# Kernel optimization log

Hardware: AMD Instinct MI355X
Metric: run time of the kernel (lower is better)

Reference implementation:

```python
import jax, jax.numpy as jnp
import numpy as np

K = 4  # neighbors per node (init kwarg)


def setup_inputs() -> dict:
    key = jax.random.key(0)
    node_features = jax.random.normal(key, (8, 4096, 256), dtype=jnp.float32)
    return {"node_features": node_features}


def reference(node_features):
    # node_features: (B, N, C)
    B, N, C = node_features.shape
    k = min(K, N - 1)
    # cosine metric: L2-normalize rows, then pairwise dot products
    fn = node_features / jnp.linalg.norm(node_features, axis=-1, keepdims=True)
    sim = jnp.einsum("bnc,bmc->bnm", fn, fn)  # (B, N, N)
    # exclude self-loops: fill diagonal with -inf
    diag = jnp.eye(N, dtype=bool)
    sim = jnp.where(diag[None, :, :], -jnp.inf, sim)
    topk_values, topk_indices = jax.lax.top_k(sim, k)  # (B, N, k)
    # edge list per batch: source i repeated k times, target = topk index
    src = jnp.broadcast_to(jnp.arange(N)[:, None], (N, k)).reshape(-1)  # (N*k,)
    src = jnp.broadcast_to(src[None, :], (B, N * k))
    tgt = topk_indices.reshape(B, N * k)
    edge_index = jnp.stack([src, tgt], axis=1)  # (B, 2, N*k)
    edge_weight = topk_values.reshape(B, N * k)  # (B, N*k)
    return edge_index, edge_weight
```

## Files before the change

### kernel.cpp

```cpp
#include <hip/hip_runtime.h>
#include <hip/hip_bf16.h>
#include <float.h>
#include <limits.h>

#define BATCH 8
#define NN    4096
#define CC    256
#define KNN_K 4
#define NKE   (NN * KNN_K)

#define MTI  64
#define NJ   64
#define NC8  8
#define NM6  6
#define BROW 264

typedef __attribute__((ext_vector_type(8))) short  bf16x8;
typedef __attribute__((ext_vector_type(4))) float  f32x4;

__device__ __forceinline__ short f2bf(float f) {
    unsigned u = __float_as_uint(f);
    return (short)((u + 0x7FFFu + ((u >> 16) & 1u)) >> 16);
}

__device__ __forceinline__ unsigned umin32(unsigned a, unsigned b) { return a < b ? a : b; }
__device__ __forceinline__ unsigned umax32(unsigned a, unsigned b) { return a > b ? a : b; }

__device__ __forceinline__ void pk_ins8(unsigned k, unsigned (&t)[NC8]) {
    #pragma unroll
    for (int s = NC8 - 1; s > 0; --s) t[s] = umax32(t[s], umin32(t[s - 1], k));
    t[0] = umax32(t[0], k);
}
__device__ __forceinline__ void pk_ins6(unsigned k, unsigned (&t)[NM6]) {
    #pragma unroll
    for (int s = NM6 - 1; s > 0; --s) t[s] = umax32(t[s], umin32(t[s - 1], k));
    t[0] = umax32(t[0], k);
}

__device__ __forceinline__ bool knn_better(float v, int j, float v2, int j2) {
    return (v > v2) || (v == v2 && j < j2);
}
__device__ __forceinline__ void knn_insert4(float v, int j, float (&tv)[4], int (&tj)[4]) {
    if (knn_better(v, j, tv[3], tj[3])) {
        tv[3] = v; tj[3] = j;
        #pragma unroll
        for (int s = 3; s > 0; --s) {
            if (knn_better(tv[s], tj[s], tv[s - 1], tj[s - 1])) {
                float fv = tv[s]; tv[s] = tv[s - 1]; tv[s - 1] = fv;
                int   fj = tj[s]; tj[s] = tj[s - 1]; tj[s - 1] = fj;
            }
        }
    }
}

__global__ void knn_prep_kernel(const float* __restrict__ x, float* __restrict__ invn,
                                ushort* __restrict__ xn, int write_bf16) {
    const int row  = blockIdx.x * 4 + (threadIdx.x >> 6);
    const int lane = threadIdx.x & 63;
    const float4 v = *(const float4*)(x + (size_t)row * CC + lane * 4);
    float ss = v.x * v.x + v.y * v.y + v.z * v.z + v.w * v.w;
    #pragma unroll
    for (int off = 32; off > 0; off >>= 1) ss += __shfl_down(ss, off, 64);
    const float inv = 1.0f / sqrtf(__shfl(ss, 0, 64));
    if (lane == 0) invn[row] = inv;
    if (write_bf16) {
        short4 s4;
        s4.x = f2bf(v.x * inv); s4.y = f2bf(v.y * inv);
        s4.z = f2bf(v.z * inv); s4.w = f2bf(v.w * inv);
        *(short4*)(xn + (size_t)row * CC + lane * 4) = s4;
    }
}

template<bool FROM_BF16>
__global__ __launch_bounds__(256, 3) void knn_main_kernel(
        const float* __restrict__ x, const float* __restrict__ invn,
        const ushort* __restrict__ xn, float* __restrict__ out,
        float* __restrict__ sval, int* __restrict__ sjid, int nh2) {
    __shared__ __align__(16) ushort Bsh[NJ * BROW];

    const int tid = threadIdx.x;
    const int b   = blockIdx.x & 7;
    const int t   = blockIdx.x >> 3;
    const int it   = nh2 ? (t >> 1) : t;
    const int half = nh2 ? (t & 1)  : 0;
    const int i0   = it * MTI;
    const int jbase = half * (NN / 2);
    const int nch   = nh2 ? (NN / NJ / 2) : (NN / NJ);

    const float*  xb   = x    + (size_t)b * NN * CC;
    const ushort* xnb  = xn   + (size_t)b * NN * CC;
    const float*  invb = invn + (size_t)b * NN;

    const int w  = tid >> 6;
    const int l  = tid & 63;
    const int lm = l & 15;
    const int q  = l >> 4;

    bf16x8 afrag[8];
    const int gi = i0 + w * 16 + lm;
    if (FROM_BF16) {
        #pragma unroll
        for (int kt = 0; kt < 8; ++kt)
            afrag[kt] = *(const bf16x8*)(xnb + (size_t)gi * CC + kt * 32 + q * 8);
    } else {
        const float vi = invb[gi];
        #pragma unroll
        for (int kt = 0; kt < 8; ++kt) {
            const float* src = xb + (size_t)gi * CC + kt * 32 + q * 8;
            const float4 f0 = *(const float4*)(src);
            const float4 f1 = *(const float4*)(src + 4);
            bf16x8 a;
            a[0] = f2bf(f0.x * vi); a[1] = f2bf(f0.y * vi);
            a[2] = f2bf(f0.z * vi); a[3] = f2bf(f0.w * vi);
            a[4] = f2bf(f1.x * vi); a[5] = f2bf(f1.y * vi);
            a[6] = f2bf(f1.z * vi); a[7] = f2bf(f1.w * vi);
            afrag[kt] = a;
        }
    }

    unsigned cl[4][NC8];
    #pragma unroll
    for (int r = 0; r < 4; ++r)
        #pragma unroll
        for (int s = 0; s < NC8; ++s) cl[r][s] = 0u;

    const int s_gc = tid & 31;
    const int s_r0 = tid >> 5;
    bf16x8 pregs[8];
    if (FROM_BF16) {
        #pragma unroll
        for (int lp = 0; lp < 8; ++lp)
            pregs[lp] = *(const bf16x8*)(xnb + (size_t)(jbase + s_r0 + 8 * lp) * CC + s_gc * 8);
    }

    for (int jt = 0; jt < nch; ++jt) {
        const int j0 = jbase + jt * NJ;
        __syncthreads();
        if (FROM_BF16) {
            #pragma unroll
            for (int lp = 0; lp < 8; ++lp)
                *(bf16x8*)(Bsh + (s_r0 + 8 * lp) * BROW + s_gc * 8) = pregs[lp];
        } else {
            #pragma unroll
            for (int lp = 0; lp < 16; ++lp) {
                const int u2 = tid + 256 * lp;
                const int row = u2 >> 6, c4 = u2 & 63;
                const float sc = invb[j0 + row];
                const float4 v = *(const float4*)(xb + (size_t)(j0 + row) * CC + c4 * 4);
                short4 s4;
                s4.x = f2bf(v.x * sc); s4.y = f2bf(v.y * sc);
                s4.z = f2bf(v.z * sc); s4.w = f2bf(v.w * sc);
                *(short4*)(Bsh + row * BROW + c4 * 4) = s4;
            }
        }
        __syncthreads();
        if (FROM_BF16 && jt + 1 < nch) {
            const int jn = jbase + (jt + 1) * NJ;
            #pragma unroll
            for (int lp = 0; lp < 8; ++lp)
                pregs[lp] = *(const bf16x8*)(xnb + (size_t)(jn + s_r0 + 8 * lp) * CC + s_gc * 8);
        }

        f32x4 acc[4];
        #pragma unroll
        for (int ct = 0; ct < 4; ++ct) acc[ct] = (f32x4){0.f, 0.f, 0.f, 0.f};
        #pragma unroll
        for (int kt = 0; kt < 8; ++kt) {
            #pragma unroll
            for (int ct = 0; ct < 4; ++ct) {
                const bf16x8 bf = *(const bf16x8*)(Bsh + (ct * 16 + lm) * BROW + kt * 32 + q * 8);
                acc[ct] = __builtin_amdgcn_mfma_f32_16x16x32_bf16(afrag[kt], bf, acc[ct], 0, 0, 0);
            }
        }

        const bool dchunk = (j0 == i0);
        #pragma unroll
        for (int ct = 0; ct < 4; ++ct) {
            const int jg  = j0 + ct * 16 + lm;
            const unsigned ivj = (unsigned)(4095 - jg);
            #pragma unroll
            for (int r = 0; r < 4; ++r) {
                unsigned pk = (__float_as_uint(acc[ct][r] + 2.0f) & 0xFFFFF000u) | ivj;
                if (dchunk && (w * 16 + q * 4 + r) == (ct * 16 + lm)) pk = 0u;
                pk_ins8(pk, cl[r]);
            }
        }
    }

    unsigned tm[4][NM6];
    #pragma unroll
    for (int r = 0; r < 4; ++r)
        #pragma unroll
        for (int s = 0; s < NM6; ++s) tm[r][s] = cl[r][s];
    #pragma unroll
    for (int m = 1; m <= 8; m <<= 1) {
        #pragma unroll
        for (int r = 0; r < 4; ++r) {
            unsigned pin[NM6];
            #pragma unroll
            for (int s = 0; s < NM6; ++s)
                pin[s] = (unsigned)__shfl_xor((int)tm[r][s], m, 64);
            #pragma unroll
            for (int s = 0; s < NM6; ++s) pk_ins6(pin[s], tm[r]);
        }
    }

    unsigned* cpk = (unsigned*)Bsh;
    __syncthreads();
    if (lm == 0) {
        #pragma unroll
        for (int r = 0; r < 4; ++r) {
            const int rt = w * 16 + q * 4 + r;
            #pragma unroll
            for (int s = 0; s < NM6; ++s) cpk[rt * NM6 + s] = tm[r][s];
        }
    }
    __syncthreads();

    const int rr   = tid & 63;
    const int slot = tid >> 6;
    const int ig   = i0 + rr;
    const float inv_i = invb[ig];
    const float* xi = xb + (size_t)ig * CC;
    const int ncand = (slot < 2) ? 2 : 1;
    const int cbase = (slot < 2) ? slot * 2 : 2 + slot;
    float rv[2]; int rj[2];
    for (int u = 0; u < ncand; ++u) {
        const int c  = cbase + u;
        const int jc = 4095 - (int)(cpk[rr * NM6 + c] & 0xFFFu);
        const float* xj = xb + (size_t)jc * CC;
        float d = 0.f;
        #pragma unroll 16
        for (int k4 = 0; k4 < 64; ++k4) {
            const float4 av = *(const float4*)(xi + k4 * 4);
            const float4 bv = *(const float4*)(xj + k4 * 4);
            d = fmaf(av.x, bv.x, d);
            d = fmaf(av.y, bv.y, d);
            d = fmaf(av.z, bv.z, d);
            d = fmaf(av.w, bv.w, d);
        }
        rv[u] = d * inv_i * invb[jc];
        rj[u] = jc;
    }

    if (nh2) {
        for (int u = 0; u < ncand; ++u) {
            const size_t o = ((size_t)(b * NN + ig) * 2 + half) * NM6 + (cbase + u);
            sval[o] = rv[u];
            sjid[o] = rj[u];
        }
        return;
    }

    float* cvl = (float*)(Bsh + 4096);
    for (int u = 0; u < ncand; ++u) cvl[rr * NM6 + (cbase + u)] = rv[u];
    __syncthreads();
    if (tid < MTI) {
        const int r = tid, ig2 = i0 + r;
        float fv[4]; int fj[4];
        #pragma unroll
        for (int s = 0; s < 4; ++s) { fv[s] = -INFINITY; fj[s] = INT_MAX; }
        for (int c = 0; c < NM6; ++c) {
            const int jc = 4095 - (int)(cpk[r * NM6 + c] & 0xFFFu);
            knn_insert4(cvl[r * NM6 + c], jc, fv, fj);
        }
        float* o_src = out + (size_t)b * 2 * NKE;
        float* o_tgt = o_src + NKE;
        float* o_w   = out + (size_t)BATCH * 2 * NKE + (size_t)b * NKE;
        #pragma unroll
        for (int s = 0; s < 4; ++s) {
            o_src[ig2 * KNN_K + s] = (float)ig2;
            o_tgt[ig2 * KNN_K + s] = (float)fj[s];
            o_w[ig2 * KNN_K + s]   = fv[s];
        }
    }
}

__global__ __launch_bounds__(256) void knn_select_kernel(
        const float* __restrict__ sval, const int* __restrict__ sjid,
        float* __restrict__ out) {
    const int row_g = blockIdx.x * 256 + threadIdx.x;
    const int bb = row_g >> 12, ig = row_g & (NN - 1);
    float fv[4]; int fj[4];
    #pragma unroll
    for (int s = 0; s < 4; ++s) { fv[s] = -INFINITY; fj[s] = INT_MAX; }
    const size_t base = (size_t)row_g * 2 * NM6;
    for (int c = 0; c < 2 * NM6; ++c)
        knn_insert4(sval[base + c], sjid[base + c], fv, fj);
    float* o_src = out + (size_t)bb * 2 * NKE;
    float* o_tgt = o_src + NKE;
    float* o_w   = out + (size_t)BATCH * 2 * NKE + (size_t)bb * NKE;
    #pragma unroll
    for (int s = 0; s < 4; ++s) {
        o_src[ig * KNN_K + s] = (float)ig;
        o_tgt[ig * KNN_K + s] = (float)fj[s];
        o_w[ig * KNN_K + s]   = fv[s];
    }
}

extern "C" void kernel_launch(void* const* d_in, const int* in_sizes, int n_in,
                              void* d_out, int out_size, void* d_ws, size_t ws_size,
                              hipStream_t stream) {
    const float* x    = (const float*)d_in[0];
    float*       out  = (float*)d_out;
    float*       invn = (float*)d_ws;
    ushort*      xn   = (ushort*)((char*)d_ws + 131072);
    char*        p2   = (char*)d_ws + 131072 + (size_t)BATCH * NN * CC * sizeof(ushort);
    float*       sval = (float*)p2;
    int*         sjid = (int*)(p2 + (size_t)BATCH * NN * 2 * NM6 * sizeof(float));
    const size_t need_xn  = 131072 + (size_t)BATCH * NN * CC * sizeof(ushort);
    const size_t need_all = need_xn + (size_t)BATCH * NN * 2 * NM6 * 8;

    if (ws_size >= need_all) {
        knn_prep_kernel<<<(BATCH * NN) / 4, 256, 0, stream>>>(x, invn, xn, 1);
        knn_main_kernel<true><<<BATCH * MTI * 2, 256, 0, stream>>>(x, invn, xn, out, sval, sjid, 1);
        knn_select_kernel<<<(BATCH * NN) / 256, 256, 0, stream>>>(sval, sjid, out);
    } else if (ws_size >= need_xn) {
        knn_prep_kernel<<<(BATCH * NN) / 4, 256, 0, stream>>>(x, invn, xn, 1);
        knn_main_kernel<true><<<BATCH * MTI, 256, 0, stream>>>(x, invn, xn, out, nullptr, nullptr, 0);
    } else {
        knn_prep_kernel<<<(BATCH * NN) / 4, 256, 0, stream>>>(x, invn, xn, 0);
        knn_main_kernel<false><<<BATCH * MTI, 256, 0, stream>>>(x, invn, xn, out, nullptr, nullptr, 0);
    }
}
```

Before: 256.4 us.

## Use 2x2 wave tiling with direct global-to-LDS loads and per-half candidate lists

Each wave now computes a 32x32 sub-tile of the 64x64 similarity block instead of 16x64. This halves the B-fragment LDS reads per MFMA by reusing each B fragment across two A row tiles. The B tile is filled with global_load_lds straight into shared memory, replacing the register prefetch and LDS store, which drops the software overlap of the next chunk's load. Each row now keeps two 6-entry candidate lists, one per column-half wave, instead of one 8-entry list. That doubles the fp32 rescoring and select work (12 or 24 candidates per row) and adds workspace traffic.

```diff
diff --git a/kernel.cpp b/kernel.cpp
--- a/kernel.cpp
+++ b/kernel.cpp
@@ -11,9 +11,9 @@
 
 #define MTI  64
 #define NJ   64
-#define NC8  8
-#define NM6  6
+#define NCD  6
 #define BROW 264
+#define NGR  2112
 
 typedef __attribute__((ext_vector_type(8))) short  bf16x8;
 typedef __attribute__((ext_vector_type(4))) float  f32x4;
@@ -26,14 +26,9 @@
 __device__ __forceinline__ unsigned umin32(unsigned a, unsigned b) { return a < b ? a : b; }
 __device__ __forceinline__ unsigned umax32(unsigned a, unsigned b) { return a > b ? a : b; }
 
-__device__ __forceinline__ void pk_ins8(unsigned k, unsigned (&t)[NC8]) {
-    #pragma unroll
-    for (int s = NC8 - 1; s > 0; --s) t[s] = umax32(t[s], umin32(t[s - 1], k));
-    t[0] = umax32(t[0], k);
-}
-__device__ __forceinline__ void pk_ins6(unsigned k, unsigned (&t)[NM6]) {
-    #pragma unroll
-    for (int s = NM6 - 1; s > 0; --s) t[s] = umax32(t[s], umin32(t[s - 1], k));
+__device__ __forceinline__ void pk_ins6(unsigned k, unsigned (&t)[NCD]) {
+    #pragma unroll
+    for (int s = NCD - 1; s > 0; --s) t[s] = umax32(t[s], umin32(t[s - 1], k));
     t[0] = umax32(t[0], k);
 }
 
@@ -95,51 +90,62 @@
     const int l  = tid & 63;
     const int lm = l & 15;
     const int q  = l >> 4;
-
-    bf16x8 afrag[8];
-    const int gi = i0 + w * 16 + lm;
-    if (FROM_BF16) {
-        #pragma unroll
-        for (int kt = 0; kt < 8; ++kt)
-            afrag[kt] = *(const bf16x8*)(xnb + (size_t)gi * CC + kt * 32 + q * 8);
-    } else {
-        const float vi = invb[gi];
-        #pragma unroll
-        for (int kt = 0; kt < 8; ++kt) {
-            const float* src = xb + (size_t)gi * CC + kt * 32 + q * 8;
-            const float4 f0 = *(const float4*)(src);
-            const float4 f1 = *(const float4*)(src + 4);
-            bf16x8 a;
-            a[0] = f2bf(f0.x * vi); a[1] = f2bf(f0.y * vi);
-            a[2] = f2bf(f0.z * vi); a[3] = f2bf(f0.w * vi);
-            a[4] = f2bf(f1.x * vi); a[5] = f2bf(f1.y * vi);
-            a[6] = f2bf(f1.z * vi); a[7] = f2bf(f1.w * vi);
-            afrag[kt] = a;
-        }
-    }
-
-    unsigned cl[4][NC8];
-    #pragma unroll
-    for (int r = 0; r < 4; ++r)
-        #pragma unroll
-        for (int s = 0; s < NC8; ++s) cl[r][s] = 0u;
-
-    const int s_gc = tid & 31;
-    const int s_r0 = tid >> 5;
-    bf16x8 pregs[8];
-    if (FROM_BF16) {
-        #pragma unroll
-        for (int lp = 0; lp < 8; ++lp)
-            pregs[lp] = *(const bf16x8*)(xnb + (size_t)(jbase + s_r0 + 8 * lp) * CC + s_gc * 8);
-    }
+    const int wr = w >> 1;
+    const int wc = w & 1;
+
+    bf16x8 afrag[2][8];
+    #pragma unroll
+    for (int rt = 0; rt < 2; ++rt) {
+        const int gi = i0 + wr * 32 + rt * 16 + lm;
+        if (FROM_BF16) {
+            #pragma unroll
+            for (int kt = 0; kt < 8; ++kt)
+                afrag[rt][kt] = *(const bf16x8*)(xnb + (size_t)gi * CC + kt * 32 + q * 8);
+        } else {
+            const float vi = invb[gi];
+            #pragma unroll
+            for (int kt = 0; kt < 8; ++kt) {
+                const float* src = xb + (size_t)gi * CC + kt * 32 + q * 8;
+                const float4 f0 = *(const float4*)(src);
+                const float4 f1 = *(const float4*)(src + 4);
+                bf16x8 a;
+                a[0] = f2bf(f0.x * vi); a[1] = f2bf(f0.y * vi);
+                a[2] = f2bf(f0.z * vi); a[3] = f2bf(f0.w * vi);
+                a[4] = f2bf(f1.x * vi); a[5] = f2bf(f1.y * vi);
+                a[6] = f2bf(f1.z * vi); a[7] = f2bf(f1.w * vi);
+                afrag[rt][kt] = a;
+            }
+        }
+    }
+
+    unsigned cl[8][NCD];
+    #pragma unroll
+    for (int li = 0; li < 8; ++li)
+        #pragma unroll
+        for (int s = 0; s < NCD; ++s) cl[li][s] = 0u;
+
+    const int r0 = (tid * 993) >> 15;
+    const int c0 = tid - r0 * 33;
 
     for (int jt = 0; jt < nch; ++jt) {
         const int j0 = jbase + jt * NJ;
         __syncthreads();
         if (FROM_BF16) {
-            #pragma unroll
-            for (int lp = 0; lp < 8; ++lp)
-                *(bf16x8*)(Bsh + (s_r0 + 8 * lp) * BROW + s_gc * 8) = pregs[lp];
+            int r = r0, c = c0;
+            #pragma unroll
+            for (int lp = 0; lp < 9; ++lp) {
+                if (lp < 8 || w == 0) {
+                    const int cc2 = (c == 32) ? 0 : c;
+                    const ushort* src = xnb + (size_t)(j0 + r) * CC + cc2 * 8;
+                    ushort* dst = Bsh + (lp * 2048 + w * 512);
+                    __builtin_amdgcn_global_load_lds(
+                        (const __attribute__((address_space(1))) unsigned int*)src,
+                        (__attribute__((address_space(3))) unsigned int*)dst,
+                        16, 0, 0);
+                }
+                c += 25; r += 7;
+                if (c >= 33) { c -= 33; ++r; }
+            }
         } else {
             #pragma unroll
             for (int lp = 0; lp < 16; ++lp) {
@@ -154,54 +160,53 @@
             }
         }
         __syncthreads();
-        if (FROM_BF16 && jt + 1 < nch) {
-            const int jn = jbase + (jt + 1) * NJ;
-            #pragma unroll
-            for (int lp = 0; lp < 8; ++lp)
-                pregs[lp] = *(const bf16x8*)(xnb + (size_t)(jn + s_r0 + 8 * lp) * CC + s_gc * 8);
-        }
-
-        f32x4 acc[4];
-        #pragma unroll
-        for (int ct = 0; ct < 4; ++ct) acc[ct] = (f32x4){0.f, 0.f, 0.f, 0.f};
+
+        f32x4 acc[2][2];
+        #pragma unroll
+        for (int rt = 0; rt < 2; ++rt)
+            #pragma unroll
+            for (int ct = 0; ct < 2; ++ct) acc[rt][ct] = (f32x4){0.f, 0.f, 0.f, 0.f};
         #pragma unroll
         for (int kt = 0; kt < 8; ++kt) {
-            #pragma unroll
-            for (int ct = 0; ct < 4; ++ct) {
-                const bf16x8 bf = *(const bf16x8*)(Bsh + (ct * 16 + lm) * BROW + kt * 32 + q * 8);
-                acc[ct] = __builtin_amdgcn_mfma_f32_16x16x32_bf16(afrag[kt], bf, acc[ct], 0, 0, 0);
-            }
+            bf16x8 bf[2];
+            #pragma unroll
+            for (int ct = 0; ct < 2; ++ct)
+                bf[ct] = *(const bf16x8*)(Bsh + (wc * 32 + ct * 16 + lm) * BROW + kt * 32 + q * 8);
+            #pragma unroll
+            for (int rt = 0; rt < 2; ++rt)
+                #pragma unroll
+                for (int ct = 0; ct < 2; ++ct)
+                    acc[rt][ct] = __builtin_amdgcn_mfma_f32_16x16x32_bf16(
+                        afrag[rt][kt], bf[ct], acc[rt][ct], 0, 0, 0);
         }
 
         const bool dchunk = (j0 == i0);
         #pragma unroll
-        for (int ct = 0; ct < 4; ++ct) {
-            const int jg  = j0 + ct * 16 + lm;
-            const unsigned ivj = (unsigned)(4095 - jg);
-            #pragma unroll
-            for (int r = 0; r < 4; ++r) {
-                unsigned pk = (__float_as_uint(acc[ct][r] + 2.0f) & 0xFFFFF000u) | ivj;
-                if (dchunk && (w * 16 + q * 4 + r) == (ct * 16 + lm)) pk = 0u;
-                pk_ins8(pk, cl[r]);
-            }
-        }
-    }
-
-    unsigned tm[4][NM6];
-    #pragma unroll
-    for (int r = 0; r < 4; ++r)
-        #pragma unroll
-        for (int s = 0; s < NM6; ++s) tm[r][s] = cl[r][s];
+        for (int ct = 0; ct < 2; ++ct) {
+            const int jl  = wc * 32 + ct * 16 + lm;
+            const unsigned ivj = (unsigned)(4095 - (j0 + jl));
+            #pragma unroll
+            for (int rt = 0; rt < 2; ++rt)
+                #pragma unroll
+                for (int reg = 0; reg < 4; ++reg) {
+                    const int rl = wr * 32 + rt * 16 + q * 4 + reg;
+                    unsigned pk = (__float_as_uint(acc[rt][ct][reg] + 2.0f) & 0xFFFFF000u) | ivj;
+                    if (dchunk && rl == jl) pk = 0u;
+                    pk_ins6(pk, cl[rt * 4 + reg]);
+                }
+        }
+    }
+
     #pragma unroll
     for (int m = 1; m <= 8; m <<= 1) {
         #pragma unroll
-        for (int r = 0; r < 4; ++r) {
-            unsigned pin[NM6];
-            #pragma unroll
-            for (int s = 0; s < NM6; ++s)
-                pin[s] = (unsigned)__shfl_xor((int)tm[r][s], m, 64);
-            #pragma unroll
-            for (int s = 0; s < NM6; ++s) pk_ins6(pin[s], tm[r]);
+        for (int li = 0; li < 8; ++li) {
+            unsigned pin[NCD];
+            #pragma unroll
+            for (int s = 0; s < NCD; ++s)
+                pin[s] = (unsigned)__shfl_xor((int)cl[li][s], m, 64);
+            #pragma unroll
+            for (int s = 0; s < NCD; ++s) pk_ins6(pin[s], cl[li]);
         }
     }
 
@@ -209,10 +214,10 @@
     __syncthreads();
     if (lm == 0) {
         #pragma unroll
-        for (int r = 0; r < 4; ++r) {
-            const int rt = w * 16 + q * 4 + r;
-            #pragma unroll
-            for (int s = 0; s < NM6; ++s) cpk[rt * NM6 + s] = tm[r][s];
+        for (int li = 0; li < 8; ++li) {
+            const int rl = wr * 32 + (li >> 2) * 16 + q * 4 + (li & 3);
+            #pragma unroll
+            for (int s = 0; s < NCD; ++s) cpk[rl * 12 + wc * 6 + s] = cl[li][s];
         }
     }
     __syncthreads();
@@ -222,12 +227,11 @@
     const int ig   = i0 + rr;
     const float inv_i = invb[ig];
     const float* xi = xb + (size_t)ig * CC;
-    const int ncand = (slot < 2) ? 2 : 1;
-    const int cbase = (slot < 2) ? slot * 2 : 2 + slot;
-    float rv[2]; int rj[2];
-    for (int u = 0; u < ncand; ++u) {
-        const int c  = cbase + u;
-        const int jc = 4095 - (int)(cpk[rr * NM6 + c] & 0xFFFu);
+    float rv[3]; int rj[3];
+    #pragma unroll
+    for (int u = 0; u < 3; ++u) {
+        const int c  = slot * 3 + u;
+        const int jc = 4095 - (int)(cpk[rr * 12 + c] & 0xFFFu);
         const float* xj = xb + (size_t)jc * CC;
         float d = 0.f;
         #pragma unroll 16
@@ -244,25 +248,27 @@
     }
 
     if (nh2) {
-        for (int u = 0; u < ncand; ++u) {
-            const size_t o = ((size_t)(b * NN + ig) * 2 + half) * NM6 + (cbase + u);
+        #pragma unroll
+        for (int u = 0; u < 3; ++u) {
+            const size_t o = ((size_t)(b * NN + ig) * 2 + half) * 12 + (slot * 3 + u);
             sval[o] = rv[u];
             sjid[o] = rj[u];
         }
         return;
     }
 
-    float* cvl = (float*)(Bsh + 4096);
-    for (int u = 0; u < ncand; ++u) cvl[rr * NM6 + (cbase + u)] = rv[u];
+    float* cvl = (float*)(Bsh + 2048);
+    #pragma unroll
+    for (int u = 0; u < 3; ++u) cvl[rr * 12 + slot * 3 + u] = rv[u];
     __syncthreads();
     if (tid < MTI) {
         const int r = tid, ig2 = i0 + r;
         float fv[4]; int fj[4];
         #pragma unroll
         for (int s = 0; s < 4; ++s) { fv[s] = -INFINITY; fj[s] = INT_MAX; }
-        for (int c = 0; c < NM6; ++c) {
-            const int jc = 4095 - (int)(cpk[r * NM6 + c] & 0xFFFu);
-            knn_insert4(cvl[r * NM6 + c], jc, fv, fj);
+        for (int c = 0; c < 12; ++c) {
+            const int jc = 4095 - (int)(cpk[r * 12 + c] & 0xFFFu);
+            knn_insert4(cvl[r * 12 + c], jc, fv, fj);
         }
         float* o_src = out + (size_t)b * 2 * NKE;
         float* o_tgt = o_src + NKE;
@@ -284,8 +290,8 @@
     float fv[4]; int fj[4];
     #pragma unroll
     for (int s = 0; s < 4; ++s) { fv[s] = -INFINITY; fj[s] = INT_MAX; }
-    const size_t base = (size_t)row_g * 2 * NM6;
-    for (int c = 0; c < 2 * NM6; ++c)
+    const size_t base = (size_t)row_g * 24;
+    for (int c = 0; c < 24; ++c)
         knn_insert4(sval[base + c], sjid[base + c], fv, fj);
     float* o_src = out + (size_t)bb * 2 * NKE;
     float* o_tgt = o_src + NKE;
@@ -307,9 +313,9 @@
     ushort*      xn   = (ushort*)((char*)d_ws + 131072);
     char*        p2   = (char*)d_ws + 131072 + (size_t)BATCH * NN * CC * sizeof(ushort);
     float*       sval = (float*)p2;
-    int*         sjid = (int*)(p2 + (size_t)BATCH * NN * 2 * NM6 * sizeof(float));
+    int*         sjid = (int*)(p2 + (size_t)BATCH * NN * 24 * sizeof(float));
     const size_t need_xn  = 131072 + (size_t)BATCH * NN * CC * sizeof(ushort);
-    const size_t need_all = need_xn + (size_t)BATCH * NN * 2 * NM6 * 8;
+    const size_t need_all = need_xn + (size_t)BATCH * NN * 24 * 8;
 
     if (ws_size >= need_all) {
         knn_prep_kernel<<<(BATCH * NN) / 4, 256, 0, stream>>>(x, invn, xn, 1);
```

Measured after the change: 432.6 us. +68.7%, slower.
